# Performance work log

Hardware: AMD Instinct MI355X
Metric: run time of the kernel (lower is better)

Reference implementation:

```python
import jax, jax.numpy as jnp
import numpy as np

N_SRNA = 20000
N_MRNA = 100000
HID = 128
E_S2M = 1_000_000
E_M2M = 2_000_000
E_LBL = 500_000
N_LAYERS = 2


def setup_inputs() -> dict:
    key = jax.random.key(0)
    ks = jax.random.split(key, 20)
    s = 0.05
    inp = {
        # edge lists (rev edge types are flips, derived inside reference)
        "s2m_src": jax.random.randint(ks[0], (E_S2M,), 0, N_SRNA),
        "s2m_dst": jax.random.randint(ks[1], (E_S2M,), 0, N_MRNA),
        "m2m_src": jax.random.randint(ks[2], (E_M2M,), 0, N_MRNA),
        "m2m_dst": jax.random.randint(ks[3], (E_M2M,), 0, N_MRNA),
        "label_src": jax.random.randint(ks[4], (E_LBL,), 0, N_SRNA),
        "label_dst": jax.random.randint(ks[5], (E_LBL,), 0, N_MRNA),
        # embeddings (node_id is arange over all nodes -> identity lookup)
        "srna_emb": jax.random.normal(ks[6], (N_SRNA, HID), jnp.float32),
        "mrna_emb": jax.random.normal(ks[7], (N_MRNA, HID), jnp.float32),
        # per-layer stacked params. SAGEConv: out = lin_l(mean_agg)+lin_r(x_dst)
        "sage_s2m_Wl": jax.random.normal(ks[8], (N_LAYERS, HID, HID), jnp.float32) * s,
        "sage_s2m_bl": jnp.zeros((N_LAYERS, HID), jnp.float32),
        "sage_s2m_Wr": jax.random.normal(ks[9], (N_LAYERS, HID, HID), jnp.float32) * s,
        "sage_rev_Wl": jax.random.normal(ks[10], (N_LAYERS, HID, HID), jnp.float32) * s,
        "sage_rev_bl": jnp.zeros((N_LAYERS, HID), jnp.float32),
        "sage_rev_Wr": jax.random.normal(ks[11], (N_LAYERS, HID, HID), jnp.float32) * s,
        # GCNConv: out = propagate(norm, x @ W) + b
        "gcn_m2m_W": jax.random.normal(ks[12], (N_LAYERS, HID, HID), jnp.float32) * s,
        "gcn_m2m_b": jnp.zeros((N_LAYERS, HID), jnp.float32),
        "gcn_rev_W": jax.random.normal(ks[13], (N_LAYERS, HID, HID), jnp.float32) * s,
        "gcn_rev_b": jnp.zeros((N_LAYERS, HID), jnp.float32),
    }
    return inp


def _sage(x_src, x_dst, src, dst, n_dst, Wl, bl, Wr):
    # PyG SAGEConv (aggr='mean', root_weight=True): lin_l(mean_msg) + lin_r(x_dst)
    agg = jax.ops.segment_sum(x_src[src], dst, num_segments=n_dst)  # [n_dst, h]
    cnt = jax.ops.segment_sum(jnp.ones((src.shape[0],), x_src.dtype), dst,
                              num_segments=n_dst)
    agg = agg / jnp.maximum(cnt, 1.0)[:, None]
    return agg @ Wl + bl + x_dst @ Wr


def _gcn(x, src, dst, n, W, b):
    # PyG GCNConv: add self-loops, sym-normalize, x @ W, propagate, + bias
    xw = x @ W  # [n, h]
    deg = jax.ops.segment_sum(jnp.ones((src.shape[0],), x.dtype), dst,
                              num_segments=n) + 1.0  # +1 self-loop
    dinv = jax.lax.rsqrt(deg)
    norm = dinv[src] * dinv[dst]  # [E]
    out = jax.ops.segment_sum(norm[:, None] * xw[src], dst, num_segments=n)
    out = out + (dinv * dinv)[:, None] * xw  # self-loop term
    return out + b


def reference(s2m_src, s2m_dst, m2m_src, m2m_dst, label_src, label_dst,
              srna_emb, mrna_emb,
              sage_s2m_Wl, sage_s2m_bl, sage_s2m_Wr,
              sage_rev_Wl, sage_rev_bl, sage_rev_Wr,
              gcn_m2m_W, gcn_m2m_b, gcn_rev_W, gcn_rev_b):
    x_s, x_m = srna_emb, mrna_emb
    for l in range(N_LAYERS):
        # HeteroConv aggr='sum' over edge types per dst node type
        m_new = _sage(x_s, x_m, s2m_src, s2m_dst, N_MRNA,
                      sage_s2m_Wl[l], sage_s2m_bl[l], sage_s2m_Wr[l])
        m_new = m_new + _gcn(x_m, m2m_src, m2m_dst, N_MRNA,
                             gcn_m2m_W[l], gcn_m2m_b[l])
        m_new = m_new + _gcn(x_m, m2m_dst, m2m_src, N_MRNA,
                             gcn_rev_W[l], gcn_rev_b[l])  # rev_similar = flip
        s_new = _sage(x_m, x_s, s2m_dst, s2m_src, N_SRNA,
                      sage_rev_Wl[l], sage_rev_bl[l], sage_rev_Wr[l])
        x_s, x_m = jax.nn.relu(s_new), jax.nn.relu(m_new)
    # Classifier: dot product over labeled (srna, mrna) pairs
    return (x_s[label_src] * x_m[label_dst]).sum(axis=-1)
```

## Files before the change

kernel.cpp:

```cpp
#include <hip/hip_runtime.h>
#include <hip/hip_fp16.h>

#define NS 20000
#define NM 100000
#define H  128
#define ES 1000000
#define EM 2000000
#define EL 500000

#define SH_M 7
#define SH_S 6
#define NB_SD 782
#define NB_SS 313
#define NB_MD 782
#define NB_MS 782
#define CAP_SD 1664
#define CAP_SS 3904
#define CAP_MD 3200
#define CAP_MS 3200
#define MAXCAP 3904
#define CHUNK 4096
#define B_SD ((ES + CHUNK - 1) / CHUNK)
#define B_SS ((ES + CHUNK - 1) / CHUNK)
#define B_MD ((EM + CHUNK - 1) / CHUNK)
#define B_MS ((EM + CHUNK - 1) / CHUNK)
#define VAL_MASK 0x1FFFF

#define MB_M (NM / 16)
#define MB_S (NS / 16)
#define APAD 136

#define P1_BLKS (B_SD + B_SS + B_MD + B_MS)
#define PB_M 12500
#define PB_S 2500
#define PB_W 768

#define SD_GBLK (NM * 16 / 256)
#define FIN_BLK ((NM + 255) / 256)

typedef _Float16 half8 __attribute__((ext_vector_type(8)));
typedef float floatx4 __attribute__((ext_vector_type(4)));

__global__ __launch_bounds__(256) void place1_prep(
        const int* __restrict__ s2m_src, const int* __restrict__ s2m_dst,
        const int* __restrict__ m2m_src, const int* __restrict__ m2m_dst,
        int* __restrict__ bc,
        unsigned int* __restrict__ p_sd, unsigned int* __restrict__ p_ss,
        unsigned int* __restrict__ p_md, unsigned int* __restrict__ p_ms,
        const float* __restrict__ m_emb, const float* __restrict__ s_emb,
        const float* __restrict__ w0, const float* __restrict__ w1,
        const float* __restrict__ w2, const float* __restrict__ w3,
        const float* __restrict__ w4, const float* __restrict__ w5,
        __half* __restrict__ xm16, __half* __restrict__ xs16,
        __half* __restrict__ wbuf) {
    __shared__ unsigned int rec[CHUNK];
    __shared__ unsigned short eb[CHUNK];
    __shared__ int cnt[1024];
    __shared__ int gbase[1024];

    int b = blockIdx.x;
    int t = threadIdx.x;

    if (b >= P1_BLKS) {
        int pb = b - P1_BLKS;
        if (pb < PB_M) {
            long long i = (long long)pb * 256 + t;
            float4 v = *(const float4*)&m_emb[i * 4];
            __half2 h0 = __floats2half2_rn(v.x, v.y);
            __half2 h1 = __floats2half2_rn(v.z, v.w);
            __half2* o = (__half2*)&xm16[i * 4];
            o[0] = h0; o[1] = h1;
        } else if (pb < PB_M + PB_S) {
            long long i = (long long)(pb - PB_M) * 256 + t;
            float4 v = *(const float4*)&s_emb[i * 4];
            __half2 h0 = __floats2half2_rn(v.x, v.y);
            __half2 h1 = __floats2half2_rn(v.z, v.w);
            __half2* o = (__half2*)&xs16[i * 4];
            o[0] = h0; o[1] = h1;
        } else {
            int idx = (pb - PB_M - PB_S) * 256 + t;
            int mat = idx / (H * H);
            int rem = idx % (H * H);
            int n = rem / H;
            int k = rem % H;
            const float* base;
            switch (mat >> 1) {
            case 0: base = w0; break; case 1: base = w1; break; case 2: base = w2; break;
            case 3: base = w3; break; case 4: base = w4; break; default: base = w5; break;
            }
            base += (size_t)(mat & 1) * H * H;
            wbuf[(size_t)mat * H * H + (size_t)n * H + k] = __float2half(base[(size_t)k * H + n]);
        }
        return;
    }

    const int *keys, *vals; int shift, cap, E, bcoff; unsigned int* pp;
    int cb;
    if (b < B_SD)                    { cb = b;                      keys = s2m_dst; vals = s2m_src; shift = SH_M; cap = CAP_SD; E = ES; bcoff = 0;     pp = p_sd; }
    else if (b < B_SD+B_SS)          { cb = b - B_SD;               keys = s2m_src; vals = s2m_dst; shift = SH_S; cap = CAP_SS; E = ES; bcoff = 16384; pp = p_ss; }
    else if (b < B_SD+B_SS+B_MD)     { cb = b - B_SD - B_SS;        keys = m2m_dst; vals = m2m_src; shift = SH_M; cap = CAP_MD; E = EM; bcoff = 32768; pp = p_md; }
    else                             { cb = b - B_SD - B_SS - B_MD; keys = m2m_src; vals = m2m_dst; shift = SH_M; cap = CAP_MS; E = EM; bcoff = 49152; pp = p_ms; }
    int* bcp = bc + bcoff;

    int e0 = cb * CHUNK;
    int nv = E - e0; if (nv > CHUNK) nv = CHUNK;

    for (int i = t; i < nv; i += 256) {
        int k = keys[e0 + i];
        int v = vals[e0 + i];
        int bkt = k >> shift;
        rec[i] = ((unsigned int)(k - (bkt << shift)) << 17) | (unsigned int)v;
        eb[i] = (unsigned short)bkt;
    }
#pragma unroll
    for (int j = 0; j < 4; ++j) cnt[t * 4 + j] = 0;
    __syncthreads();
    for (int i = t; i < nv; i += 256) atomicAdd(&cnt[eb[i]], 1);
    __syncthreads();
#pragma unroll
    for (int j = 0; j < 4; ++j) {
        int bk = t * 4 + j;
        int c = cnt[bk];
        if (c > 0) {
            gbase[bk] = atomicAdd(&bcp[bk << 4], c);
            cnt[bk] = 0;
        }
    }
    __syncthreads();
    for (int i = t; i < nv; i += 256) {
        int bk = eb[i];
        int pos = atomicAdd(&cnt[bk], 1);
        int o = gbase[bk] + pos;
        if (o < cap) pp[(size_t)bk * cap + o] = rec[i];
    }
}

__global__ __launch_bounds__(256) void place2_fused(
        const int* __restrict__ bc,
        const unsigned int* __restrict__ p_sd, const unsigned int* __restrict__ p_ss,
        const unsigned int* __restrict__ p_md, const unsigned int* __restrict__ p_ms,
        int* __restrict__ adj_sd, int* __restrict__ adj_ss,
        int* __restrict__ adj_md, int* __restrict__ adj_ms,
        int* __restrict__ off_sd, int* __restrict__ off_ss,
        int* __restrict__ off_md, int* __restrict__ off_ms,
        int* __restrict__ cnt_sd, int* __restrict__ cnt_ss,
        int* __restrict__ cnt_md, int* __restrict__ cnt_ms) {
    __shared__ unsigned int lp[MAXCAP];
    __shared__ int hist[128], cur[128], sbuf[128];
    int b = blockIdx.x;
    int c, lb;
    if (b < NB_SD)                    { c = 0; lb = b; }
    else if (b < NB_SD+NB_SS)         { c = 1; lb = b - NB_SD; }
    else if (b < NB_SD+NB_SS+NB_MD)   { c = 2; lb = b - NB_SD - NB_SS; }
    else                              { c = 3; lb = b - NB_SD - NB_SS - NB_MD; }
    const unsigned int* pp; int *adj, *offp, *cntp; int shift, cap, n;
    switch (c) {
    case 0:  pp = p_sd; adj = adj_sd; offp = off_sd; cntp = cnt_sd; shift = SH_M; cap = CAP_SD; n = NM; break;
    case 1:  pp = p_ss; adj = adj_ss; offp = off_ss; cntp = cnt_ss; shift = SH_S; cap = CAP_SS; n = NS; break;
    case 2:  pp = p_md; adj = adj_md; offp = off_md; cntp = cnt_md; shift = SH_M; cap = CAP_MD; n = NM; break;
    default: pp = p_ms; adj = adj_ms; offp = off_ms; cntp = cnt_ms; shift = SH_M; cap = CAP_MS; n = NM; break;
    }
    int t = threadIdx.x;
    int k = bc[c * 16384 + (lb << 4)];
    if (k > cap) k = cap;
    int base = lb << shift;
    int npb = 1 << shift;
    int bb = lb * cap;
    for (int i = t; i < k; i += 256) lp[i] = pp[(size_t)lb * cap + i];
    if (t < npb) hist[t] = 0;
    __syncthreads();
    for (int i = t; i < k; i += 256) atomicAdd(&hist[lp[i] >> 17], 1);
    __syncthreads();
    int v = (t < npb) ? hist[t] : 0;
    if (t < 128) sbuf[t] = v;
    __syncthreads();
    for (int d = 1; d < 128; d <<= 1) {
        int x = 0;
        if (t >= d && t < 128) x = sbuf[t - d];
        __syncthreads();
        if (t >= d && t < 128) sbuf[t] += x;
        __syncthreads();
    }
    if (t < npb) {
        int excl = sbuf[t] - v;
        cur[t] = excl;
        int node = base + t;
        if (node < n) { offp[node] = bb + excl; cntp[node] = v; }
    }
    __syncthreads();
    for (int i = t; i < k; i += 256) {
        unsigned int p = lp[i];
        int pos = atomicAdd(&cur[p >> 17], 1);
        adj[(size_t)bb + pos] = (int)(p & VAL_MASK);
    }
}

__device__ __forceinline__ void gacc_plain(const __half* __restrict__ X,
                                           const int* __restrict__ adj,
                                           int o, int k, int c, float (&acc)[8]) {
    int j = 0;
    for (; j + 8 <= k; j += 8) {
        int s0 = adj[o+j+0], s1 = adj[o+j+1], s2 = adj[o+j+2], s3 = adj[o+j+3];
        int s4 = adj[o+j+4], s5 = adj[o+j+5], s6 = adj[o+j+6], s7 = adj[o+j+7];
        half8 v0 = *(const half8*)(X + (size_t)s0 * H + c);
        half8 v1 = *(const half8*)(X + (size_t)s1 * H + c);
        half8 v2 = *(const half8*)(X + (size_t)s2 * H + c);
        half8 v3 = *(const half8*)(X + (size_t)s3 * H + c);
        half8 v4 = *(const half8*)(X + (size_t)s4 * H + c);
        half8 v5 = *(const half8*)(X + (size_t)s5 * H + c);
        half8 v6 = *(const half8*)(X + (size_t)s6 * H + c);
        half8 v7 = *(const half8*)(X + (size_t)s7 * H + c);
#pragma unroll
        for (int i = 0; i < 8; ++i)
            acc[i] += (float)v0[i] + (float)v1[i] + (float)v2[i] + (float)v3[i]
                    + (float)v4[i] + (float)v5[i] + (float)v6[i] + (float)v7[i];
    }
    for (; j + 4 <= k; j += 4) {
        int s0 = adj[o+j+0], s1 = adj[o+j+1], s2 = adj[o+j+2], s3 = adj[o+j+3];
        half8 v0 = *(const half8*)(X + (size_t)s0 * H + c);
        half8 v1 = *(const half8*)(X + (size_t)s1 * H + c);
        half8 v2 = *(const half8*)(X + (size_t)s2 * H + c);
        half8 v3 = *(const half8*)(X + (size_t)s3 * H + c);
#pragma unroll
        for (int i = 0; i < 8; ++i)
            acc[i] += (float)v0[i] + (float)v1[i] + (float)v2[i] + (float)v3[i];
    }
    for (; j < k; ++j) {
        int s = adj[o + j];
        half8 v = *(const half8*)(X + (size_t)s * H + c);
#pragma unroll
        for (int i = 0; i < 8; ++i) acc[i] += (float)v[i];
    }
}

__device__ __forceinline__ void gacc_weighted(const __half* __restrict__ X,
                                              const int* __restrict__ adj,
                                              const float* __restrict__ dinv,
                                              int o, int k, int c, float (&acc)[8]) {
    int j = 0;
    for (; j + 8 <= k; j += 8) {
        int s0 = adj[o+j+0], s1 = adj[o+j+1], s2 = adj[o+j+2], s3 = adj[o+j+3];
        int s4 = adj[o+j+4], s5 = adj[o+j+5], s6 = adj[o+j+6], s7 = adj[o+j+7];
        float d0 = dinv[s0], d1 = dinv[s1], d2 = dinv[s2], d3 = dinv[s3];
        float d4 = dinv[s4], d5 = dinv[s5], d6 = dinv[s6], d7 = dinv[s7];
        half8 v0 = *(const half8*)(X + (size_t)s0 * H + c);
        half8 v1 = *(const half8*)(X + (size_t)s1 * H + c);
        half8 v2 = *(const half8*)(X + (size_t)s2 * H + c);
        half8 v3 = *(const half8*)(X + (size_t)s3 * H + c);
        half8 v4 = *(const half8*)(X + (size_t)s4 * H + c);
        half8 v5 = *(const half8*)(X + (size_t)s5 * H + c);
        half8 v6 = *(const half8*)(X + (size_t)s6 * H + c);
        half8 v7 = *(const half8*)(X + (size_t)s7 * H + c);
#pragma unroll
        for (int i = 0; i < 8; ++i)
            acc[i] += d0 * (float)v0[i] + d1 * (float)v1[i] + d2 * (float)v2[i] + d3 * (float)v3[i]
                    + d4 * (float)v4[i] + d5 * (float)v5[i] + d6 * (float)v6[i] + d7 * (float)v7[i];
    }
    for (; j + 4 <= k; j += 4) {
        int s0 = adj[o+j+0], s1 = adj[o+j+1], s2 = adj[o+j+2], s3 = adj[o+j+3];
        float d0 = dinv[s0], d1 = dinv[s1], d2 = dinv[s2], d3 = dinv[s3];
        half8 v0 = *(const half8*)(X + (size_t)s0 * H + c);
        half8 v1 = *(const half8*)(X + (size_t)s1 * H + c);
        half8 v2 = *(const half8*)(X + (size_t)s2 * H + c);
        half8 v3 = *(const half8*)(X + (size_t)s3 * H + c);
#pragma unroll
        for (int i = 0; i < 8; ++i)
            acc[i] += d0 * (float)v0[i] + d1 * (float)v1[i] + d2 * (float)v2[i] + d3 * (float)v3[i];
    }
    for (; j < k; ++j) {
        int s = adj[o + j];
        float ds = dinv[s];
        half8 v = *(const half8*)(X + (size_t)s * H + c);
#pragma unroll
        for (int i = 0; i < 8; ++i) acc[i] += ds * (float)v[i];
    }
}

__device__ __forceinline__ void st_h8(__half* p, const float (&a)[8]) {
    half8 h;
#pragma unroll
    for (int i = 0; i < 8; ++i) h[i] = (_Float16)a[i];
    *(half8*)p = h;
}

__global__ __launch_bounds__(256) void sage_sd_fin(
        const __half* __restrict__ xs_in,
        const int* __restrict__ off_sd, const int* __restrict__ cnt_sd,
        const int* __restrict__ adj_sd,
        const int* __restrict__ c_md, const int* __restrict__ c_ms,
        __half* __restrict__ SA, float* __restrict__ dvf, float* __restrict__ dvr) {
    int b = blockIdx.x, t = threadIdx.x;
    if (b >= SD_GBLK) {
        int i = (b - SD_GBLK) * 256 + t;
        if (i < NM) {
            dvf[i] = rsqrtf((float)c_md[i] + 1.0f);
            dvr[i] = rsqrtf((float)c_ms[i] + 1.0f);
        }
        return;
    }
    long long gid = (long long)b * 256 + t;
    int g = (int)(gid >> 4);
    int c = ((int)gid & 15) * 8;
    float acc[8] = {0.f,0.f,0.f,0.f,0.f,0.f,0.f,0.f};
    int k = cnt_sd[g];
    gacc_plain(xs_in, adj_sd, off_sd[g], k, c, acc);
    float ic = 1.0f / fmaxf((float)k, 1.0f);
#pragma unroll
    for (int i = 0; i < 8; ++i) acc[i] *= ic;
    st_h8(SA + (size_t)g * H + c, acc);
}

__global__ __launch_bounds__(256) void fused_layer(
        const __half* __restrict__ xs_in, const __half* __restrict__ xm_in,
        const __half* __restrict__ SA,
        const int* __restrict__ off_md, const int* __restrict__ cnt_md, const int* __restrict__ adj_md,
        const int* __restrict__ off_ms, const int* __restrict__ cnt_ms, const int* __restrict__ adj_ms,
        const int* __restrict__ off_ss, const int* __restrict__ cnt_ss, const int* __restrict__ adj_ss,
        const float* __restrict__ dvf, const float* __restrict__ dvr,
        const __half* __restrict__ wbuf,
        const float* __restrict__ bl, const float* __restrict__ gb,
        const float* __restrict__ grb, const float* __restrict__ bls,
        __half* __restrict__ xm_out, __half* __restrict__ xs_out, int layer)
{
    __shared__ __half At[4][16][APAD];
    const int t = threadIdx.x;
    const int grp = t >> 4;
    const int c = (t & 15) * 8;
    const size_t HH = (size_t)H * H;
    const bool isM = (int)blockIdx.x < MB_M;

    if (isM) {
        const int r = blockIdx.x * 16 + grp;
        *(half8*)&At[0][grp][c] = *(const half8*)(SA + (size_t)r * H + c);
        half8 self = *(const half8*)(xm_in + (size_t)r * H + c);
        *(half8*)&At[1][grp][c] = self;
        float acc[8] = {0.f,0.f,0.f,0.f,0.f,0.f,0.f,0.f};
        gacc_weighted(xm_in, adj_md, dvf, off_md[r], cnt_md[r], c, acc);
        float dd = dvf[r], s2 = dd * dd;
#pragma unroll
        for (int i = 0; i < 8; ++i) acc[i] = dd * acc[i] + s2 * (float)self[i];
        st_h8(&At[2][grp][c], acc);
#pragma unroll
        for (int i = 0; i < 8; ++i) acc[i] = 0.f;
        gacc_weighted(xm_in, adj_ms, dvr, off_ms[r], cnt_ms[r], c, acc);
        dd = dvr[r]; s2 = dd * dd;
#pragma unroll
        for (int i = 0; i < 8; ++i) acc[i] = dd * acc[i] + s2 * (float)self[i];
        st_h8(&At[3][grp][c], acc);
        __syncthreads();
        const int w = t >> 6, lane = t & 63, quad = lane >> 4, nlo = lane & 15;
        floatx4 o0, o1;
        o0[0]=0.f;o0[1]=0.f;o0[2]=0.f;o0[3]=0.f;
        o1[0]=0.f;o1[1]=0.f;o1[2]=0.f;o1[3]=0.f;
        const int t0 = 2 * w, t1 = 2 * w + 1;
#pragma unroll
        for (int seg = 0; seg < 4; ++seg) {
            const __half* Wt = wbuf + (size_t)(seg * 2 + layer) * HH;
#pragma unroll
            for (int k0 = 0; k0 < 128; k0 += 32) {
                half8 a = *(const half8*)&At[seg][nlo][k0 + quad * 8];
                half8 b0 = *(const half8*)(Wt + (size_t)(t0 * 16 + nlo) * H + k0 + quad * 8);
                half8 b1 = *(const half8*)(Wt + (size_t)(t1 * 16 + nlo) * H + k0 + quad * 8);
                o0 = __builtin_amdgcn_mfma_f32_16x16x32_f16(a, b0, o0, 0, 0, 0);
                o1 = __builtin_amdgcn_mfma_f32_16x16x32_f16(a, b1, o1, 0, 0, 0);
            }
        }
        const int bm = blockIdx.x * 16;
#pragma unroll
        for (int u = 0; u < 2; ++u) {
            floatx4 oo = u ? o1 : o0;
            int col = (2 * w + u) * 16 + nlo;
            float bias = bl[col] + gb[col] + grb[col];
#pragma unroll
            for (int i = 0; i < 4; ++i) {
                int rr = bm + quad * 4 + i;
                xm_out[(size_t)rr * H + col] = __float2half(fmaxf(oo[i] + bias, 0.f));
            }
        }
    } else {
        const int blk = (int)blockIdx.x - MB_M;
        const int r = blk * 16 + grp;
        float acc[8] = {0.f,0.f,0.f,0.f,0.f,0.f,0.f,0.f};
        int k = cnt_ss[r];
        gacc_plain(xm_in, adj_ss, off_ss[r], k, c, acc);
        float ic = 1.0f / fmaxf((float)k, 1.0f);
#pragma unroll
        for (int i = 0; i < 8; ++i) acc[i] *= ic;
        st_h8(&At[0][grp][c], acc);
        *(half8*)&At[1][grp][c] = *(const half8*)(xs_in + (size_t)r * H + c);
        __syncthreads();
        const int w = t >> 6, lane = t & 63, quad = lane >> 4, nlo = lane & 15;
        floatx4 o0, o1;
        o0[0]=0.f;o0[1]=0.f;o0[2]=0.f;o0[3]=0.f;
        o1[0]=0.f;o1[1]=0.f;o1[2]=0.f;o1[3]=0.f;
        const int t0 = 2 * w, t1 = 2 * w + 1;
#pragma unroll
        for (int seg = 0; seg < 2; ++seg) {
            const __half* Wt = wbuf + (size_t)((4 + seg) * 2 + layer) * HH;
#pragma unroll
            for (int k0 = 0; k0 < 128; k0 += 32) {
                half8 a = *(const half8*)&At[seg][nlo][k0 + quad * 8];
                half8 b0 = *(const half8*)(Wt + (size_t)(t0 * 16 + nlo) * H + k0 + quad * 8);
                half8 b1 = *(const half8*)(Wt + (size_t)(t1 * 16 + nlo) * H + k0 + quad * 8);
                o0 = __builtin_amdgcn_mfma_f32_16x16x32_f16(a, b0, o0, 0, 0, 0);
                o1 = __builtin_amdgcn_mfma_f32_16x16x32_f16(a, b1, o1, 0, 0, 0);
            }
        }
        const int bm = blk * 16;
#pragma unroll
        for (int u = 0; u < 2; ++u) {
            floatx4 oo = u ? o1 : o0;
            int col = (2 * w + u) * 16 + nlo;
            float bias = bls[col];
#pragma unroll
            for (int i = 0; i < 4; ++i) {
                int rr = bm + quad * 4 + i;
                xs_out[(size_t)rr * H + col] = __float2half(fmaxf(oo[i] + bias, 0.f));
            }
        }
    }
}

__global__ void classify(const __half* __restrict__ xs16, const __half* __restrict__ xm16,
                         const int* __restrict__ ls, const int* __restrict__ ld,
                         float* __restrict__ out, int P) {
    long long gid = (long long)blockIdx.x * blockDim.x + threadIdx.x;
    int p = (int)(gid >> 4);
    if (p >= P) return;
    int lane = (int)gid & 15;
    int a = ls[p], b = ld[p];
    half8 u = *(const half8*)(xs16 + (size_t)a * H + lane * 8);
    half8 v = *(const half8*)(xm16 + (size_t)b * H + lane * 8);
    float s = 0.f;
#pragma unroll
    for (int i = 0; i < 8; ++i) s += (float)u[i] * (float)v[i];
    for (int off = 8; off > 0; off >>= 1) s += __shfl_down(s, off, 16);
    if (lane == 0) out[p] = s;
}

extern "C" void kernel_launch(void* const* d_in, const int* in_sizes, int n_in,
                              void* d_out, int out_size, void* d_ws, size_t ws_size,
                              hipStream_t stream) {
    const int* s2m_src = (const int*)d_in[0];
    const int* s2m_dst = (const int*)d_in[1];
    const int* m2m_src = (const int*)d_in[2];
    const int* m2m_dst = (const int*)d_in[3];
    const int* lbl_src = (const int*)d_in[4];
    const int* lbl_dst = (const int*)d_in[5];
    const float* s_emb = (const float*)d_in[6];
    const float* m_emb = (const float*)d_in[7];
    const float* Wl_s2m = (const float*)d_in[8];
    const float* bl_s2m = (const float*)d_in[9];
    const float* Wr_s2m = (const float*)d_in[10];
    const float* Wl_rev = (const float*)d_in[11];
    const float* bl_rev = (const float*)d_in[12];
    const float* Wr_rev = (const float*)d_in[13];
    const float* gW  = (const float*)d_in[14];
    const float* gb  = (const float*)d_in[15];
    const float* grW = (const float*)d_in[16];
    const float* grb = (const float*)d_in[17];

    __half* hws = (__half*)d_ws;
    size_t ho = 0;
    __half* xm16_a = hws + ho; ho += (size_t)NM * H;
    __half* xm16_b = hws + ho; ho += (size_t)NM * H;
    __half* xs16_a = hws + ho; ho += (size_t)NS * H;
    __half* xs16_b = hws + ho; ho += (size_t)NS * H;
    __half* scratch = hws + ho; ho += (size_t)(3 * NM + NS) * H;
    __half* wbuf = hws + ho; ho += (size_t)12 * H * H;

    float* fws = (float*)(hws + ho);
    size_t fo = 0;
    float* dvf = fws + fo; fo += NM;
    float* dvr = fws + fo; fo += NM;

    int* ip = (int*)(fws + fo);
    size_t io = 0;
    int* off_sd = ip + io; io += NM;
    int* off_ss = ip + io; io += NS;
    int* off_md = ip + io; io += NM;
    int* off_ms = ip + io; io += NM;
    int* cnt_sd = ip + io; io += NM;
    int* cnt_ss = ip + io; io += NS;
    int* cnt_md = ip + io; io += NM;
    int* cnt_ms = ip + io; io += NM;
    int* bc     = ip + io; io += 4 * 16384;
    int* adj_sd = ip + io; io += NB_SD * CAP_SD;
    int* adj_ss = ip + io; io += NB_SS * CAP_SS;
    int* adj_md = ip + io; io += NB_MD * CAP_MD;
    int* adj_ms = ip + io; io += NB_MS * CAP_MS;

    unsigned int* p_sd = (unsigned int*)scratch;
    unsigned int* p_ss = p_sd + (size_t)NB_SD * CAP_SD;
    unsigned int* p_md = p_ss + (size_t)NB_SS * CAP_SS;
    unsigned int* p_ms = p_md + (size_t)NB_MD * CAP_MD;

    __half* SA = scratch;

    hipMemsetAsync(bc, 0, 4 * 16384 * sizeof(int), stream);
    place1_prep<<<P1_BLKS + PB_M + PB_S + PB_W, 256, 0, stream>>>(
        s2m_src, s2m_dst, m2m_src, m2m_dst, bc, p_sd, p_ss, p_md, p_ms,
        m_emb, s_emb, Wl_s2m, Wr_s2m, gW, grW, Wl_rev, Wr_rev,
        xm16_a, xs16_a, wbuf);
    place2_fused<<<NB_SD + NB_SS + NB_MD + NB_MS, 256, 0, stream>>>(
        bc, p_sd, p_ss, p_md, p_ms,
        adj_sd, adj_ss, adj_md, adj_ms,
        off_sd, off_ss, off_md, off_ms,
        cnt_sd, cnt_ss, cnt_md, cnt_ms);

    const __half* xin_m = xm16_a;
    const __half* xin_s = xs16_a;
    __half* xout_m = xm16_b;
    __half* xout_s = xs16_b;

    for (int l = 0; l < 2; ++l) {
        const size_t bo = (size_t)l * H;
        sage_sd_fin<<<SD_GBLK + FIN_BLK, 256, 0, stream>>>(
            xin_s, off_sd, cnt_sd, adj_sd, cnt_md, cnt_ms, SA, dvf, dvr);
        fused_layer<<<MB_M + MB_S, 256, 0, stream>>>(
            xin_s, xin_m, SA,
            off_md, cnt_md, adj_md,
            off_ms, cnt_ms, adj_ms,
            off_ss, cnt_ss, adj_ss,
            dvf, dvr, wbuf,
            bl_s2m + bo, gb + bo, grb + bo, bl_rev + bo,
            xout_m, xout_s, l);
        const __half* tm = xin_m; xin_m = xout_m; xout_m = (__half*)tm;
        const __half* ts = xin_s; xin_s = xout_s; xout_s = (__half*)ts;
    }

    classify<<<(int)(((long long)EL * 16 + 255) / 256), 256, 0, stream>>>(
        xin_s, xin_m, lbl_src, lbl_dst, (float*)d_out, EL);
}
```

Measured before the change: 825.1 us.

## Degree-sort node worklists so fused layer blocks group rows with similar degree

Adds histogram, scan and scatter kernels that bucket mRNA and sRNA nodes by their total in-degree, in descending order, and build permutation worklists. fused_layer then reads its 16 rows per block from these worklists instead of taking consecutive node ids. The goal is to cut intra-block load imbalance, where 16-lane groups wait on the highest-degree row, and to schedule heavy blocks first. In exchange it adds three small kernel launches, scattered output rows, and less locality on the self and SA row reads.

```diff
diff --git a/kernel.cpp b/kernel.cpp
--- a/kernel.cpp
+++ b/kernel.cpp
@@ -37,6 +37,9 @@
 
 #define SD_GBLK (NM * 16 / 256)
 #define FIN_BLK ((NM + 255) / 256)
+
+#define HB_M ((NM + 255) / 256)
+#define HB_S ((NS + 255) / 256)
 
 typedef _Float16 half8 __attribute__((ext_vector_type(8)));
 typedef float floatx4 __attribute__((ext_vector_type(4)));
@@ -195,6 +198,69 @@
     }
 }
 
+__global__ void bin_hist(const int* __restrict__ c_md, const int* __restrict__ c_ms,
+                         const int* __restrict__ c_ss, int* __restrict__ binCnt) {
+    __shared__ int lb[64];
+    int b = blockIdx.x, t = threadIdx.x;
+    if (t < 64) lb[t] = 0;
+    __syncthreads();
+    if (b < HB_M) {
+        int i = b * 256 + t;
+        if (i < NM) {
+            int bin = (c_md[i] + c_ms[i] + 7) >> 3; if (bin > 63) bin = 63;
+            atomicAdd(&lb[bin], 1);
+        }
+    } else {
+        int i = (b - HB_M) * 256 + t;
+        if (i < NS) {
+            int bin = (c_ss[i] + 7) >> 3; if (bin > 63) bin = 63;
+            atomicAdd(&lb[bin], 1);
+        }
+    }
+    __syncthreads();
+    int base = (b < HB_M) ? 0 : 64;
+    if (t < 64 && lb[t] > 0) atomicAdd(&binCnt[base + t], lb[t]);
+}
+
+__global__ void bin_scan(const int* __restrict__ binCnt, int* __restrict__ binBase) {
+    int t = threadIdx.x;
+    int s = t >> 6, b2 = t & 63;
+    int off = 0;
+    for (int q = 63; q > b2; --q) off += binCnt[s * 64 + q];
+    binBase[t] = off;
+}
+
+__global__ void bin_scatter(const int* __restrict__ c_md, const int* __restrict__ c_ms,
+                            const int* __restrict__ c_ss, int* __restrict__ binBase,
+                            int* __restrict__ wl_m, int* __restrict__ wl_s) {
+    __shared__ int lc[64], lb[64];
+    int b = blockIdx.x, t = threadIdx.x;
+    if (t < 64) lc[t] = 0;
+    __syncthreads();
+    int bin = 0, pos = 0; bool valid = false; int i = -1;
+    if (b < HB_M) {
+        i = b * 256 + t;
+        if (i < NM) {
+            bin = (c_md[i] + c_ms[i] + 7) >> 3; if (bin > 63) bin = 63;
+            pos = atomicAdd(&lc[bin], 1); valid = true;
+        }
+    } else {
+        i = (b - HB_M) * 256 + t;
+        if (i < NS) {
+            bin = (c_ss[i] + 7) >> 3; if (bin > 63) bin = 63;
+            pos = atomicAdd(&lc[bin], 1); valid = true;
+        }
+    }
+    __syncthreads();
+    int base = (b < HB_M) ? 0 : 64;
+    if (t < 64 && lc[t] > 0) lb[t] = atomicAdd(&binBase[base + t], lc[t]);
+    __syncthreads();
+    if (valid) {
+        if (b < HB_M) wl_m[lb[bin] + pos] = i;
+        else          wl_s[lb[bin] + pos] = i;
+    }
+}
+
 __device__ __forceinline__ void gacc_plain(const __half* __restrict__ X,
                                            const int* __restrict__ adj,
                                            int o, int k, int c, float (&acc)[8]) {
@@ -316,6 +382,7 @@
         const int* __restrict__ off_md, const int* __restrict__ cnt_md, const int* __restrict__ adj_md,
         const int* __restrict__ off_ms, const int* __restrict__ cnt_ms, const int* __restrict__ adj_ms,
         const int* __restrict__ off_ss, const int* __restrict__ cnt_ss, const int* __restrict__ adj_ss,
+        const int* __restrict__ wl_m, const int* __restrict__ wl_s,
         const float* __restrict__ dvf, const float* __restrict__ dvr,
         const __half* __restrict__ wbuf,
         const float* __restrict__ bl, const float* __restrict__ gb,
@@ -323,6 +390,7 @@
         __half* __restrict__ xm_out, __half* __restrict__ xs_out, int layer)
 {
     __shared__ __half At[4][16][APAD];
+    __shared__ int wlr[16];
     const int t = threadIdx.x;
     const int grp = t >> 4;
     const int c = (t & 15) * 8;
@@ -330,7 +398,8 @@
     const bool isM = (int)blockIdx.x < MB_M;
 
     if (isM) {
-        const int r = blockIdx.x * 16 + grp;
+        const int r = wl_m[blockIdx.x * 16 + grp];
+        if ((t & 15) == 0) wlr[grp] = r;
         *(half8*)&At[0][grp][c] = *(const half8*)(SA + (size_t)r * H + c);
         half8 self = *(const half8*)(xm_in + (size_t)r * H + c);
         *(half8*)&At[1][grp][c] = self;
@@ -365,7 +434,6 @@
                 o1 = __builtin_amdgcn_mfma_f32_16x16x32_f16(a, b1, o1, 0, 0, 0);
             }
         }
-        const int bm = blockIdx.x * 16;
 #pragma unroll
         for (int u = 0; u < 2; ++u) {
             floatx4 oo = u ? o1 : o0;
@@ -373,13 +441,14 @@
             float bias = bl[col] + gb[col] + grb[col];
 #pragma unroll
             for (int i = 0; i < 4; ++i) {
-                int rr = bm + quad * 4 + i;
+                int rr = wlr[quad * 4 + i];
                 xm_out[(size_t)rr * H + col] = __float2half(fmaxf(oo[i] + bias, 0.f));
             }
         }
     } else {
         const int blk = (int)blockIdx.x - MB_M;
-        const int r = blk * 16 + grp;
+        const int r = wl_s[blk * 16 + grp];
+        if ((t & 15) == 0) wlr[grp] = r;
         float acc[8] = {0.f,0.f,0.f,0.f,0.f,0.f,0.f,0.f};
         int k = cnt_ss[r];
         gacc_plain(xm_in, adj_ss, off_ss[r], k, c, acc);
@@ -406,7 +475,6 @@
                 o1 = __builtin_amdgcn_mfma_f32_16x16x32_f16(a, b1, o1, 0, 0, 0);
             }
         }
-        const int bm = blk * 16;
 #pragma unroll
         for (int u = 0; u < 2; ++u) {
             floatx4 oo = u ? o1 : o0;
@@ -414,7 +482,7 @@
             float bias = bls[col];
 #pragma unroll
             for (int i = 0; i < 4; ++i) {
-                int rr = bm + quad * 4 + i;
+                int rr = wlr[quad * 4 + i];
                 xs_out[(size_t)rr * H + col] = __float2half(fmaxf(oo[i] + bias, 0.f));
             }
         }
@@ -485,6 +553,10 @@
     int* cnt_md = ip + io; io += NM;
     int* cnt_ms = ip + io; io += NM;
     int* bc     = ip + io; io += 4 * 16384;
+    int* binCnt  = ip + io; io += 128;
+    int* binBase = ip + io; io += 128;
+    int* wl_m   = ip + io; io += NM;
+    int* wl_s   = ip + io; io += NS;
     int* adj_sd = ip + io; io += NB_SD * CAP_SD;
     int* adj_ss = ip + io; io += NB_SS * CAP_SS;
     int* adj_md = ip + io; io += NB_MD * CAP_MD;
@@ -497,7 +569,7 @@
 
     __half* SA = scratch;
 
-    hipMemsetAsync(bc, 0, 4 * 16384 * sizeof(int), stream);
+    hipMemsetAsync(bc, 0, (4 * 16384 + 128) * sizeof(int), stream);
     place1_prep<<<P1_BLKS + PB_M + PB_S + PB_W, 256, 0, stream>>>(
         s2m_src, s2m_dst, m2m_src, m2m_dst, bc, p_sd, p_ss, p_md, p_ms,
         m_emb, s_emb, Wl_s2m, Wr_s2m, gW, grW, Wl_rev, Wr_rev,
@@ -508,6 +580,10 @@
         off_sd, off_ss, off_md, off_ms,
         cnt_sd, cnt_ss, cnt_md, cnt_ms);
 
+    bin_hist<<<HB_M + HB_S, 256, 0, stream>>>(cnt_md, cnt_ms, cnt_ss, binCnt);
+    bin_scan<<<1, 128, 0, stream>>>(binCnt, binBase);
+    bin_scatter<<<HB_M + HB_S, 256, 0, stream>>>(cnt_md, cnt_ms, cnt_ss, binBase, wl_m, wl_s);
+
     const __half* xin_m = xm16_a;
     const __half* xin_s = xs16_a;
     __half* xout_m = xm16_b;
@@ -522,6 +598,7 @@
             off_md, cnt_md, adj_md,
             off_ms, cnt_ms, adj_ms,
             off_ss, cnt_ss, adj_ss,
+            wl_m, wl_s,
             dvf, dvr, wbuf,
             bl_s2m + bo, gb + bo, grb + bo, bl_rev + bo,
             xout_m, xout_s, l);
```

New measurement: 854.5 us. +3.6%, slower.
